# Performance work log

Hardware: AMD Instinct MI355X
Metric: run time of the kernel (lower is better)

Reference implementation:

```python
import jax, jax.numpy as jnp
import numpy as np

# hyperparams (match init_kwargs)
B, T, DV, DJ, L = 32, 256, 1024, 512, 20
K, S, LAYERS = 4, 2, 3
LAM = 4.0            # lambda_softmax used inside frame_by_word attention
MARGIN = 0.1         # opt.global_margin
EPS_BN = 1e-5
EPS_COS = 1e-8


def _bn(x):
    # training-mode BatchNorm1d(affine=False): per-channel stats over (batch, length)
    m = x.mean(axis=(0, 2), keepdims=True)
    v = ((x - m) ** 2).mean(axis=(0, 2), keepdims=True)
    return (x - m) / jnp.sqrt(v + EPS_BN)


def _conv1d(x, w, b, stride):
    # x: [N, Cin, L], w: [Cout, Cin, K], padding=0
    y = jax.lax.conv_general_dilated(x, w, (stride,), 'VALID',
                                     dimension_numbers=('NCH', 'OIH', 'NCH'))
    return y + b[None, :, None]


def setup_inputs() -> dict:
    key = jax.random.key(0)
    ks = jax.random.split(key, 10)
    inp = {
        'video': jax.random.normal(ks[0], (B, T, DV), jnp.float32),
        'words': jax.random.normal(ks[1], (B, L, DJ), jnp.float32),
        'w_masks': jnp.ones((B, L), jnp.float32),
        'conv0_w': jax.random.normal(ks[2], (DJ, DV, K), jnp.float32) * 0.02,
        'conv0_b': jnp.zeros((DJ,), jnp.float32),
        'conv1_w': jax.random.normal(ks[3], (DJ, DJ, K), jnp.float32) * 0.02,
        'conv1_b': jnp.zeros((DJ,), jnp.float32),
        'conv2_w': jax.random.normal(ks[4], (DJ, DJ, K), jnp.float32) * 0.02,
        'conv2_b': jnp.zeros((DJ,), jnp.float32),
        'conv1d_w': jax.random.normal(ks[5], (DJ, DJ, 1), jnp.float32) * 0.02,
        'conv1d_b': jnp.zeros((DJ,), jnp.float32),
    }
    return inp


def reference(video, words, w_masks, conv0_w, conv0_b, conv1_w, conv1_b,
              conv2_w, conv2_b, conv1d_w, conv1d_b):
    # --- conv/batchnorm feature extraction ---
    x = _bn(video.transpose(0, 2, 1))                     # [b, DV, T]
    feats = []
    for w_, b_ in ((conv0_w, conv0_b), (conv1_w, conv1_b), (conv2_w, conv2_b)):
        x = jax.nn.relu(_conv1d(x, w_, b_, S))
        feats.append(x)
    v = jnp.concatenate(feats, axis=-1)                   # [b, DJ, T']
    v = _conv1d(v, conv1d_w, conv1d_b, 1)
    v = _bn(v).transpose(0, 2, 1)                         # [b, T', DJ]
    w = _bn(words.transpose(0, 2, 1)).transpose(0, 2, 1)  # [b, L, DJ]

    # --- batched frame-by-word cross-attention over all (sentence i, video j) pairs ---
    att = jnp.einsum('jtd,ild->ijtl', v, w) * LAM         # [b_i, b_j, T', L]
    mask = (w_masks > 0.5)[:, None, None, :]
    att = jax.nn.softmax(jnp.where(mask, att, -1e9), axis=-1)
    v_s = jnp.einsum('ijtl,ild->ijtd', att, w)            # [b_i, b_j, T', DJ]

    # cosine similarity along feature dim
    num = jnp.einsum('jtd,ijtd->ijt', v, v_s)
    vn = jnp.maximum(jnp.linalg.norm(v, axis=-1), EPS_COS)[None]     # [1, b_j, T']
    vsn = jnp.maximum(jnp.linalg.norm(v_s, axis=-1), EPS_COS)        # [b_i, b_j, T']
    sim = num / (vn * vsn)                                # [b_i, b_j, T']

    b = sim.shape[0]
    idx = jnp.arange(b)
    positive_map = sim[idx, idx]                          # [b, T']
    scores = sim.max(axis=-1)                             # [b_i, b_j]

    # --- diag margin ranking loss ---
    dg = jnp.diagonal(scores)
    cost_s = jnp.clip(MARGIN + scores - dg[:, None], 0.0)
    cost_im = jnp.clip(MARGIN + scores - dg[None, :], 0.0)
    I = jnp.eye(b, dtype=bool)
    cost_s = jnp.where(I, 0.0, cost_s)
    cost_im = jnp.where(I, 0.0, cost_im)
    loss = cost_s.sum() / b + cost_im.sum() / b
    return loss, positive_map
```

## Files before the change

### kernel.cpp

```cpp
#include <hip/hip_runtime.h>
#include <math.h>

#define B_   32
#define T_   256
#define DV_  1024
#define DJ_  512
#define L_   20
#define T0_  127
#define T1_  62
#define T2_  30
#define TP_  219
#define LAM_ 4.0f
#define MARGIN_ 0.1f

typedef __attribute__((ext_vector_type(8))) short short8;
typedef __attribute__((ext_vector_type(4))) float f32x4;

static __device__ __forceinline__ unsigned short f2bf(float f) {
  union { float f; unsigned u; } v; v.f = f;
  unsigned r = v.u + 0x7fff + ((v.u >> 16) & 1);
  return (unsigned short)(r >> 16);
}

struct ushort4_t { unsigned short x, y, z, w; };

#define GLOAD_LDS16(gp, lp)                                                      \
  __builtin_amdgcn_global_load_lds(                                              \
      (const __attribute__((address_space(1))) void*)(gp),                       \
      (__attribute__((address_space(3))) void*)(lp), 16, 0, 0)

__global__ void reorder_all_k(const float* __restrict__ c0w, const float* __restrict__ c1w,
                              const float* __restrict__ c2w, const float* __restrict__ pww,
                              unsigned short* __restrict__ W0, unsigned short* __restrict__ W1,
                              unsigned short* __restrict__ W2, unsigned short* __restrict__ Wp) {
  int bid = blockIdx.x;
  if (bid < 2048) {
    int idx = bid * 256 + threadIdx.x;
    int co = idx >> 10, ci = idx & 1023;
    float4 w = *reinterpret_cast<const float4*>(c0w + (size_t)idx * 4);
    unsigned short* d = W0 + (size_t)co * 4096 + ci;
    d[0] = f2bf(w.x); d[1024] = f2bf(w.y); d[2048] = f2bf(w.z); d[3072] = f2bf(w.w);
  } else if (bid < 3072) {
    int idx = (bid - 2048) * 256 + threadIdx.x;
    int co = idx >> 9, ci = idx & 511;
    float4 w = *reinterpret_cast<const float4*>(c1w + (size_t)idx * 4);
    unsigned short* d = W1 + (size_t)co * 2048 + ci;
    d[0] = f2bf(w.x); d[512] = f2bf(w.y); d[1024] = f2bf(w.z); d[1536] = f2bf(w.w);
  } else if (bid < 4096) {
    int idx = (bid - 3072) * 256 + threadIdx.x;
    int co = idx >> 9, ci = idx & 511;
    float4 w = *reinterpret_cast<const float4*>(c2w + (size_t)idx * 4);
    unsigned short* d = W2 + (size_t)co * 2048 + ci;
    d[0] = f2bf(w.x); d[512] = f2bf(w.y); d[1024] = f2bf(w.z); d[1536] = f2bf(w.w);
  } else {
    int idx = (bid - 4096) * 256 + threadIdx.x;
    float4 v = *reinterpret_cast<const float4*>(pww + (size_t)idx * 4);
    ushort4_t h = { f2bf(v.x), f2bf(v.y), f2bf(v.z), f2bf(v.w) };
    reinterpret_cast<ushort4_t*>(Wp)[idx] = h;
  }
}

__global__ void stats1_k(const float* __restrict__ x, float* __restrict__ part,
                         int C, int rows, int rpg, int cpgShift) {
  int cpg  = 1 << cpgShift;
  int c4   = threadIdx.x & (cpg - 1);
  int rsub = threadIdx.x >> cpgShift;
  int nsub = 256 >> cpgShift;
  int r0 = blockIdx.x * rpg + rsub;
  int r1 = min(blockIdx.x * rpg + rpg, rows);
  float4 s = {0.f,0.f,0.f,0.f}, q = {0.f,0.f,0.f,0.f};
  for (int r = r0; r < r1; r += nsub) {
    float4 v = *reinterpret_cast<const float4*>(&x[(size_t)r * C + c4 * 4]);
    s.x += v.x; s.y += v.y; s.z += v.z; s.w += v.w;
    q.x += v.x*v.x; q.y += v.y*v.y; q.z += v.z*v.z; q.w += v.w*v.w;
  }
  float* ps = part + ((size_t)blockIdx.x * nsub + rsub) * 2 * C;
  reinterpret_cast<float4*>(ps)[c4] = s;
  reinterpret_cast<float4*>(ps + C)[c4] = q;
}

__global__ void stats2_k(const float* __restrict__ part, float* __restrict__ ms,
                         int C, int ng, float inv_n) {
  __shared__ float4 sS[8][33], sQ[8][33];
  int c4l = threadIdx.x & 31;
  int gs  = threadIdx.x >> 5;
  int c4  = blockIdx.x * 32 + c4l;
  float4 s = {0.f,0.f,0.f,0.f}, q = {0.f,0.f,0.f,0.f};
  for (int g = gs; g < ng; g += 8) {
    const float4* ps = reinterpret_cast<const float4*>(part + (size_t)g * 2 * C);
    float4 a = ps[c4];
    float4 b = ps[(C >> 2) + c4];
    s.x += a.x; s.y += a.y; s.z += a.z; s.w += a.w;
    q.x += b.x; q.y += b.y; q.z += b.z; q.w += b.w;
  }
  sS[gs][c4l] = s; sQ[gs][c4l] = q;
  __syncthreads();
  if (gs == 0) {
    float4 S = sS[0][c4l], Q = sQ[0][c4l];
#pragma unroll
    for (int k = 1; k < 8; ++k) {
      float4 a = sS[k][c4l], b = sQ[k][c4l];
      S.x += a.x; S.y += a.y; S.z += a.z; S.w += a.w;
      Q.x += b.x; Q.y += b.y; Q.z += b.z; Q.w += b.w;
    }
    int c = c4 * 4;
    float m0 = S.x * inv_n, m1 = S.y * inv_n, m2 = S.z * inv_n, m3 = S.w * inv_n;
    ms[c+0] = m0; ms[C+c+0] = rsqrtf(Q.x * inv_n - m0*m0 + 1e-5f);
    ms[c+1] = m1; ms[C+c+1] = rsqrtf(Q.y * inv_n - m1*m1 + 1e-5f);
    ms[c+2] = m2; ms[C+c+2] = rsqrtf(Q.z * inv_n - m2*m2 + 1e-5f);
    ms[c+3] = m3; ms[C+c+3] = rsqrtf(Q.w * inv_n - m3*m3 + 1e-5f);
  }
}

__global__ void vid_bn_cast_k(const float* __restrict__ video,
                              const float* __restrict__ ms,
                              unsigned short* __restrict__ vbf) {
  int i4 = blockIdx.x * 256 + threadIdx.x;
  float4 v = reinterpret_cast<const float4*>(video)[i4];
  int c = (i4 & 255) * 4;
  v.x = (v.x - ms[c+0]) * ms[1024+c+0];
  v.y = (v.y - ms[c+1]) * ms[1024+c+1];
  v.z = (v.z - ms[c+2]) * ms[1024+c+2];
  v.w = (v.w - ms[c+3]) * ms[1024+c+3];
  ushort4_t h = { f2bf(v.x), f2bf(v.y), f2bf(v.z), f2bf(v.w) };
  reinterpret_cast<ushort4_t*>(vbf)[i4] = h;
}

template<bool RELU, bool BIAS, bool OUT_BF16, bool PARTIAL>
__global__ __launch_bounds__(256) void mfma_gemm_k(
    const unsigned short* __restrict__ xin, const unsigned short* __restrict__ Wr,
    const float* __restrict__ bias, void* __restrict__ out,
    int b_stride, int row_off, int row_t_stride,
    int To, int M, int t_off_out, int ldout, int Ktot, int Kloc)
{
  __shared__ __align__(16) short As[2][64 * 32];
  __shared__ __align__(16) short Bs[2][64 * 32];

  const int tid  = threadIdx.x;
  const int lane = tid & 63;
  const int wv   = tid >> 6;
  const int wr   = wv >> 1;
  const int wc   = wv & 1;
  const int mbase = blockIdx.x * 64;
  const int nbase = blockIdx.y * 64;
  const int kstart = PARTIAL ? blockIdx.z * Kloc : 0;

  const int srow = tid >> 2;
  const int sb   = (((tid & 3) ^ ((srow ^ (srow >> 2)) & 3))) * 8;
  int ma = min(mbase + srow, M - 1);
  int b0 = ma / To, t0 = ma % To;
  const unsigned short* agp = xin + (size_t)b0 * b_stride + row_off
                              + (size_t)t0 * row_t_stride + sb + kstart;
  const unsigned short* bgp = Wr + (size_t)(nbase + srow) * Ktot + sb + kstart;

  f32x4 acc[2][2] = {};
  const int nsteps = Kloc >> 5;

#define STAGE(buf, k0)                                        \
  do {                                                        \
    GLOAD_LDS16(agp + (k0), &As[buf][wv * 512]);              \
    GLOAD_LDS16(bgp + (k0), &Bs[buf][wv * 512]);              \
  } while (0)

  STAGE(0, 0);
  __syncthreads();

  const int rsw   = (lane ^ (lane >> 2)) & 3;
  const int chunk = ((lane >> 4) ^ rsw) * 8;
  const int a_off = (wr * 32 + (lane & 15)) * 32 + chunk;
  const int b_off = (wc * 32 + (lane & 15)) * 32 + chunk;

  for (int s = 0; s < nsteps; ++s) {
    const int nb = s & 1;
    if (s + 1 < nsteps) STAGE(nb ^ 1, (s + 1) * 32);

    const short* Ab = &As[nb][a_off];
    const short* Bb = &Bs[nb][b_off];
    short8 af0 = *reinterpret_cast<const short8*>(Ab);
    short8 af1 = *reinterpret_cast<const short8*>(Ab + 512);
    short8 bf0 = *reinterpret_cast<const short8*>(Bb);
    short8 bf1 = *reinterpret_cast<const short8*>(Bb + 512);

    acc[0][0] = __builtin_amdgcn_mfma_f32_16x16x32_bf16(af0, bf0, acc[0][0], 0, 0, 0);
    acc[0][1] = __builtin_amdgcn_mfma_f32_16x16x32_bf16(af0, bf1, acc[0][1], 0, 0, 0);
    acc[1][0] = __builtin_amdgcn_mfma_f32_16x16x32_bf16(af1, bf0, acc[1][0], 0, 0, 0);
    acc[1][1] = __builtin_amdgcn_mfma_f32_16x16x32_bf16(af1, bf1, acc[1][1], 0, 0, 0);

    __syncthreads();
  }
#undef STAGE

  const int cl = lane & 15, rh = lane >> 4;
#pragma unroll
  for (int fm = 0; fm < 2; ++fm) {
#pragma unroll
    for (int fn = 0; fn < 2; ++fn) {
      int col = nbase + wc * 32 + fn * 16 + cl;
      float bv = BIAS ? bias[col] : 0.f;
      f32x4 v = acc[fm][fn];
#pragma unroll
      for (int r = 0; r < 4; ++r) {
        int m = mbase + wr * 32 + fm * 16 + rh * 4 + r;
        if (m < M) {
          if (PARTIAL) {
            float* pout = (float*)out + (size_t)blockIdx.z * ((size_t)M * ldout);
            pout[(size_t)m * ldout + col] = v[r];
          } else {
            int b = m / To, to = m % To;
            float x = v[r] + bv;
            if (RELU) x = fmaxf(x, 0.f);
            size_t oi = ((size_t)b * TP_ + t_off_out + to) * (size_t)ldout + col;
            if (OUT_BF16) ((unsigned short*)out)[oi] = f2bf(x);
            else          ((float*)out)[oi] = x;
          }
        }
      }
    }
  }
}

template<int S>
__global__ void reduce_conv_k(const float* __restrict__ part, const float* __restrict__ bias,
                              unsigned short* __restrict__ outb,
                              int M, int To, int t_off_out) {
  int idx = blockIdx.x * 256 + threadIdx.x;
  int m = idx >> 7, n4 = idx & 127;
  if (m >= M) return;
  size_t off = (size_t)m * 512 + n4 * 4;
  float4 a = *reinterpret_cast<const float4*>(part + off);
#pragma unroll
  for (int s = 1; s < S; ++s) {
    float4 b = *reinterpret_cast<const float4*>(part + (size_t)s * M * 512 + off);
    a.x += b.x; a.y += b.y; a.z += b.z; a.w += b.w;
  }
  float4 bv = *reinterpret_cast<const float4*>(bias + n4 * 4);
  a.x = fmaxf(a.x + bv.x, 0.f);
  a.y = fmaxf(a.y + bv.y, 0.f);
  a.z = fmaxf(a.z + bv.z, 0.f);
  a.w = fmaxf(a.w + bv.w, 0.f);
  int b_ = m / To, to = m % To;
  ushort4_t h = { f2bf(a.x), f2bf(a.y), f2bf(a.z), f2bf(a.w) };
  reinterpret_cast<ushort4_t*>(outb + ((size_t)b_ * TP_ + t_off_out + to) * 512)[n4] = h;
}

__global__ void v2_norm_vn_k(float* __restrict__ v2, const float* __restrict__ ms,
                             unsigned short* __restrict__ v2bf, float* __restrict__ vn) {
  int r = blockIdx.x, t = threadIdx.x;
  float* row = v2 + (size_t)r * DJ_;
  unsigned short* brow = v2bf + (size_t)r * DJ_;
  float ss = 0.f;
#pragma unroll
  for (int h = 0; h < 2; ++h) {
    int c4 = t + h * 64;
    float4 v = reinterpret_cast<float4*>(row)[c4];
    int c = c4 * 4;
    v.x = (v.x - ms[c+0]) * ms[DJ_+c+0];
    v.y = (v.y - ms[c+1]) * ms[DJ_+c+1];
    v.z = (v.z - ms[c+2]) * ms[DJ_+c+2];
    v.w = (v.w - ms[c+3]) * ms[DJ_+c+3];
    reinterpret_cast<float4*>(row)[c4] = v;
    ushort4_t h4 = { f2bf(v.x), f2bf(v.y), f2bf(v.z), f2bf(v.w) };
    reinterpret_cast<ushort4_t*>(brow)[c4] = h4;
    ss += v.x*v.x + v.y*v.y + v.z*v.z + v.w*v.w;
  }
#pragma unroll
  for (int o = 32; o; o >>= 1) ss += __shfl_down(ss, o, 64);
  if (t == 0) vn[r] = sqrtf(ss);
}

__global__ void wnorm_k(const float* __restrict__ words, const float* __restrict__ ms,
                        float* __restrict__ wbn, unsigned short* __restrict__ wbnb) {
  int idx = blockIdx.x * 256 + threadIdx.x;
  if (idx >= (B_ * L_ * DJ_) / 4) return;
  int c = (idx & 127) * 4;
  float4 v = reinterpret_cast<const float4*>(words)[idx];
  v.x = (v.x - ms[c+0]) * ms[DJ_+c+0];
  v.y = (v.y - ms[c+1]) * ms[DJ_+c+1];
  v.z = (v.z - ms[c+2]) * ms[DJ_+c+2];
  v.w = (v.w - ms[c+3]) * ms[DJ_+c+3];
  reinterpret_cast<float4*>(wbn)[idx] = v;
  ushort4_t h = { f2bf(v.x), f2bf(v.y), f2bf(v.z), f2bf(v.w) };
  reinterpret_cast<ushort4_t*>(wbnb)[idx] = h;
}

__global__ void gram_k(const float* __restrict__ wbn, float* __restrict__ G) {
  __shared__ float sw[L_ * 516];
  int i = blockIdx.x, tid = threadIdx.x;
  for (int idx = tid; idx < L_ * DJ_; idx += 256) {
    int l = idx >> 9, d = idx & 511;
    sw[l * 516 + d] = wbn[(size_t)i * L_ * DJ_ + idx];
  }
  __syncthreads();
  for (int p = tid; p < L_ * L_; p += 256) {
    int l = p / L_, l2 = p % L_;
    const float4* a = reinterpret_cast<const float4*>(&sw[l * 516]);
    const float4* b = reinterpret_cast<const float4*>(&sw[l2 * 516]);
    float acc = 0.f;
    for (int d4 = 0; d4 < 128; ++d4) {
      float4 av = a[d4], bv = b[d4];
      acc += av.x*bv.x + av.y*bv.y + av.z*bv.z + av.w*bv.w;
    }
    G[i * 400 + p] = acc;
  }
}

__global__ __launch_bounds__(256) void sim_k(
    const float* __restrict__ A, const float* __restrict__ G,
    const float* __restrict__ vn, const float* __restrict__ wmask,
    float* __restrict__ pos, float* __restrict__ scores) {
  int j = blockIdx.x, i = blockIdx.y;
  __shared__ float sG[400];
  __shared__ float sm[20];
  __shared__ float red[4];
  int tid = threadIdx.x;
  for (int p = tid; p < 400; p += 256) sG[p] = G[i * 400 + p];
  if (tid < 20) sm[tid] = wmask[i * 20 + tid];
  __syncthreads();

  float simv = -1e30f;
  if (tid < TP_) {
    const float* ar = A + ((size_t)j * TP_ + tid) * 640 + i * 20;
    float a[20], p[20];
    float mx = -1e30f;
#pragma unroll
    for (int l = 0; l < 20; ++l) {
      a[l] = ar[l];
      float lg = (sm[l] > 0.5f) ? LAM_ * a[l] : -1e9f;
      p[l] = lg;
      mx = fmaxf(mx, lg);
    }
    float Z = 0.f;
#pragma unroll
    for (int l = 0; l < 20; ++l) { p[l] = __expf(p[l] - mx); Z += p[l]; }
    float invZ = 1.f / Z, num = 0.f;
#pragma unroll
    for (int l = 0; l < 20; ++l) { p[l] *= invZ; num += p[l] * a[l]; }
    float q2 = 0.f;
#pragma unroll
    for (int l = 0; l < 20; ++l) {
      float gi = 0.f;
#pragma unroll
      for (int l2 = 0; l2 < 20; ++l2) gi += sG[l * 20 + l2] * p[l2];
      q2 += p[l] * gi;
    }
    float vnv = fmaxf(vn[(size_t)j * TP_ + tid], 1e-8f);
    float vsnv = fmaxf(sqrtf(q2), 1e-8f);
    simv = num / (vnv * vsnv);
    if (i == j) pos[i * TP_ + tid] = simv;
  }
  float mv = simv;
#pragma unroll
  for (int o = 32; o; o >>= 1) mv = fmaxf(mv, __shfl_down(mv, o, 64));
  if ((tid & 63) == 0) red[tid >> 6] = mv;
  __syncthreads();
  if (tid == 0)
    scores[i * 32 + j] = fmaxf(fmaxf(red[0], red[1]), fmaxf(red[2], red[3]));
}

__global__ void loss_k(const float* __restrict__ scores, float* __restrict__ out) {
  __shared__ float red[16];
  int tid = threadIdx.x;
  int i = tid >> 5, j = tid & 31;
  float s = scores[tid];
  float dgi = scores[i * 32 + i], dgj = scores[j * 32 + j];
  float c = 0.f;
  if (i != j)
    c = fmaxf(0.f, MARGIN_ + s - dgi) + fmaxf(0.f, MARGIN_ + s - dgj);
#pragma unroll
  for (int o = 32; o; o >>= 1) c += __shfl_down(c, o, 64);
  if ((tid & 63) == 0) red[tid >> 6] = c;
  __syncthreads();
  if (tid == 0) {
    float t = 0.f;
    for (int w = 0; w < 16; ++w) t += red[w];
    out[0] = t / 32.f;
  }
}

extern "C" void kernel_launch(void* const* d_in, const int* in_sizes, int n_in,
                              void* d_out, int out_size, void* d_ws, size_t ws_size,
                              hipStream_t stream) {
  const float* video = (const float*)d_in[0];
  const float* words = (const float*)d_in[1];
  const float* wmask = (const float*)d_in[2];
  const float* c0w = (const float*)d_in[3];
  const float* c0b = (const float*)d_in[4];
  const float* c1w = (const float*)d_in[5];
  const float* c1b = (const float*)d_in[6];
  const float* c2w = (const float*)d_in[7];
  const float* c2b = (const float*)d_in[8];
  const float* pww = (const float*)d_in[9];
  const float* pwb = (const float*)d_in[10];
  float* out = (float*)d_out;
  float* ws  = (float*)d_ws;

  float*          W0r    = ws;
  float*          W1r    = W0r + 1048576;
  float*          W2r    = W1r + 524288;
  float*          Wpw    = W2r + 524288;
  float*          AMvbf  = Wpw + 131072;
  float*          vcatb  = AMvbf + 4485120;
  float*          Pbuf   = vcatb + 1794048;
  float*          v2     = Pbuf;
  float*          v2bfp  = v2 + 3588096;
  float*          wbn    = v2bfp + 1794048;
  float*          wbnbp  = wbn + 327680;
  float*          G      = wbnbp + 163840;
  float*          vn     = G + 12800;
  float*          scores = vn + 7008;
  float*          vpart  = scores + 1024;
  float*          vms    = vpart + 1048576;
  float*          v2part = vms + 2048;
  float*          v2ms   = v2part + 897024;
  float*          wpart  = v2ms + 1024;
  float*          wms    = wpart + 81920;

  unsigned short* W0     = (unsigned short*)W0r;
  unsigned short* W1     = (unsigned short*)W1r;
  unsigned short* W2     = (unsigned short*)W2r;
  unsigned short* Wp     = (unsigned short*)Wpw;
  unsigned short* vbf    = (unsigned short*)AMvbf;
  float*          Amat   = AMvbf;
  unsigned short* vcb    = (unsigned short*)vcatb;
  unsigned short* v2bf   = (unsigned short*)v2bfp;
  unsigned short* wbnb   = (unsigned short*)wbnbp;

  reorder_all_k<<<4352, 256, 0, stream>>>(c0w, c1w, c2w, pww, W0, W1, W2, Wp);

  stats1_k<<<512, 256, 0, stream>>>(video, vpart, 1024, 8192, 16, 8);
  stats2_k<<<8, 256, 0, stream>>>(vpart, vms, 1024, 512, 1.f / 8192.f);
  vid_bn_cast_k<<<8192, 256, 0, stream>>>(video, vms, vbf);

  mfma_gemm_k<false, false, false, true><<<dim3(64, 8, 4), 256, 0, stream>>>(
      vbf, W0, nullptr, Pbuf, 262144, 0, 2048, T0_, 32 * T0_, 0, 512, 4096, 1024);
  reduce_conv_k<4><<<2032, 256, 0, stream>>>(Pbuf, c0b, vcb, 32 * T0_, T0_, 0);
  mfma_gemm_k<false, false, false, true><<<dim3(31, 8, 4), 256, 0, stream>>>(
      vcb, W1, nullptr, Pbuf, 112128, 0, 1024, T1_, 32 * T1_, 0, 512, 2048, 512);
  reduce_conv_k<4><<<992, 256, 0, stream>>>(Pbuf, c1b, vcb, 32 * T1_, T1_, T0_);
  mfma_gemm_k<false, false, false, true><<<dim3(15, 8, 8), 256, 0, stream>>>(
      vcb, W2, nullptr, Pbuf, 112128, 65024, 1024, T2_, 32 * T2_, 0, 512, 2048, 256);
  reduce_conv_k<8><<<480, 256, 0, stream>>>(Pbuf, c2b, vcb, 32 * T2_, T2_, T0_ + T1_);

  mfma_gemm_k<false, true, false, false><<<dim3(110, 8), 256, 0, stream>>>(
      vcb, Wp, pwb, v2, 112128, 0, 512, TP_, 32 * TP_, 0, 512, 512, 512);

  stats1_k<<<438, 256, 0, stream>>>(v2, v2part, 512, 7008, 16, 7);
  stats2_k<<<4, 256, 0, stream>>>(v2part, v2ms, 512, 876, 1.f / 7008.f);
  v2_norm_vn_k<<<7008, 64, 0, stream>>>(v2, v2ms, v2bf, vn);

  stats1_k<<<40, 256, 0, stream>>>(words, wpart, 512, 640, 16, 7);
  stats2_k<<<4, 256, 0, stream>>>(wpart, wms, 512, 80, 1.f / 640.f);
  wnorm_k<<<(81920 + 255) / 256, 256, 0, stream>>>(words, wms, wbn, wbnb);
  gram_k<<<32, 256, 0, stream>>>(wbn, G);

  mfma_gemm_k<false, false, false, false><<<dim3(110, 10), 256, 0, stream>>>(
      v2bf, wbnb, nullptr, Amat, 112128, 0, 512, TP_, 32 * TP_, 0, 640, 512, 512);

  sim_k<<<dim3(32, 32), 256, 0, stream>>>(Amat, G, vn, wmask, out + 1, scores);
  loss_k<<<1, 1024, 0, stream>>>(scores, out);
}
```

Before: 245.8 us.

## Enlarge MFMA GEMM tiles to 128x128 with 4x4 fragments per wave

```diff
diff --git a/kernel.cpp b/kernel.cpp
--- a/kernel.cpp
+++ b/kernel.cpp
@@ -133,42 +133,50 @@
     int b_stride, int row_off, int row_t_stride,
     int To, int M, int t_off_out, int ldout, int Ktot, int Kloc)
 {
-  __shared__ __align__(16) short As[2][64 * 32];
-  __shared__ __align__(16) short Bs[2][64 * 32];
+  __shared__ __align__(16) short As[2][128 * 32];
+  __shared__ __align__(16) short Bs[2][128 * 32];
 
   const int tid  = threadIdx.x;
   const int lane = tid & 63;
   const int wv   = tid >> 6;
   const int wr   = wv >> 1;
   const int wc   = wv & 1;
-  const int mbase = blockIdx.x * 64;
-  const int nbase = blockIdx.y * 64;
+  const int mbase = blockIdx.x * 128;
+  const int nbase = blockIdx.y * 128;
   const int kstart = PARTIAL ? blockIdx.z * Kloc : 0;
 
   const int srow = tid >> 2;
   const int sb   = (((tid & 3) ^ ((srow ^ (srow >> 2)) & 3))) * 8;
-  int ma = min(mbase + srow, M - 1);
-  int b0 = ma / To, t0 = ma % To;
-  const unsigned short* agp = xin + (size_t)b0 * b_stride + row_off
-                              + (size_t)t0 * row_t_stride + sb + kstart;
-  const unsigned short* bgp = Wr + (size_t)(nbase + srow) * Ktot + sb + kstart;
-
-  f32x4 acc[2][2] = {};
+  int ma0 = min(mbase + srow,      M - 1);
+  int ma1 = min(mbase + 64 + srow, M - 1);
+  int ba0 = ma0 / To, ta0 = ma0 % To;
+  int ba1 = ma1 / To, ta1 = ma1 % To;
+  const unsigned short* agp0 = xin + (size_t)ba0 * b_stride + row_off
+                               + (size_t)ta0 * row_t_stride + sb + kstart;
+  const unsigned short* agp1 = xin + (size_t)ba1 * b_stride + row_off
+                               + (size_t)ta1 * row_t_stride + sb + kstart;
+  const unsigned short* bgp0 = Wr + (size_t)(nbase + srow) * Ktot + sb + kstart;
+  const unsigned short* bgp1 = Wr + (size_t)(nbase + 64 + srow) * Ktot + sb + kstart;
+
+  f32x4 acc[4][4] = {};
   const int nsteps = Kloc >> 5;
 
 #define STAGE(buf, k0)                                        \
   do {                                                        \
-    GLOAD_LDS16(agp + (k0), &As[buf][wv * 512]);              \
-    GLOAD_LDS16(bgp + (k0), &Bs[buf][wv * 512]);              \
+    GLOAD_LDS16(agp0 + (k0), &As[buf][wv * 512]);             \
+    GLOAD_LDS16(agp1 + (k0), &As[buf][2048 + wv * 512]);      \
+    GLOAD_LDS16(bgp0 + (k0), &Bs[buf][wv * 512]);             \
+    GLOAD_LDS16(bgp1 + (k0), &Bs[buf][2048 + wv * 512]);      \
   } while (0)
 
   STAGE(0, 0);
   __syncthreads();
 
-  const int rsw   = (lane ^ (lane >> 2)) & 3;
+  const int l15   = lane & 15;
+  const int rsw   = (l15 ^ (l15 >> 2)) & 3;
   const int chunk = ((lane >> 4) ^ rsw) * 8;
-  const int a_off = (wr * 32 + (lane & 15)) * 32 + chunk;
-  const int b_off = (wc * 32 + (lane & 15)) * 32 + chunk;
+  const int a_off = (wr * 64 + l15) * 32 + chunk;
+  const int b_off = (wc * 64 + l15) * 32 + chunk;
 
   for (int s = 0; s < nsteps; ++s) {
     const int nb = s & 1;
@@ -176,15 +184,17 @@
 
     const short* Ab = &As[nb][a_off];
     const short* Bb = &Bs[nb][b_off];
-    short8 af0 = *reinterpret_cast<const short8*>(Ab);
-    short8 af1 = *reinterpret_cast<const short8*>(Ab + 512);
-    short8 bf0 = *reinterpret_cast<const short8*>(Bb);
-    short8 bf1 = *reinterpret_cast<const short8*>(Bb + 512);
-
-    acc[0][0] = __builtin_amdgcn_mfma_f32_16x16x32_bf16(af0, bf0, acc[0][0], 0, 0, 0);
-    acc[0][1] = __builtin_amdgcn_mfma_f32_16x16x32_bf16(af0, bf1, acc[0][1], 0, 0, 0);
-    acc[1][0] = __builtin_amdgcn_mfma_f32_16x16x32_bf16(af1, bf0, acc[1][0], 0, 0, 0);
-    acc[1][1] = __builtin_amdgcn_mfma_f32_16x16x32_bf16(af1, bf1, acc[1][1], 0, 0, 0);
+    short8 af[4], bf[4];
+#pragma unroll
+    for (int f = 0; f < 4; ++f) {
+      af[f] = *reinterpret_cast<const short8*>(Ab + f * 512);
+      bf[f] = *reinterpret_cast<const short8*>(Bb + f * 512);
+    }
+#pragma unroll
+    for (int fm = 0; fm < 4; ++fm)
+#pragma unroll
+      for (int fn = 0; fn < 4; ++fn)
+        acc[fm][fn] = __builtin_amdgcn_mfma_f32_16x16x32_bf16(af[fm], bf[fn], acc[fm][fn], 0, 0, 0);
 
     __syncthreads();
   }
@@ -192,15 +202,15 @@
 
   const int cl = lane & 15, rh = lane >> 4;
 #pragma unroll
-  for (int fm = 0; fm < 2; ++fm) {
-#pragma unroll
-    for (int fn = 0; fn < 2; ++fn) {
-      int col = nbase + wc * 32 + fn * 16 + cl;
+  for (int fm = 0; fm < 4; ++fm) {
+#pragma unroll
+    for (int fn = 0; fn < 4; ++fn) {
+      int col = nbase + wc * 64 + fn * 16 + cl;
       float bv = BIAS ? bias[col] : 0.f;
       f32x4 v = acc[fm][fn];
 #pragma unroll
       for (int r = 0; r < 4; ++r) {
-        int m = mbase + wr * 32 + fm * 16 + rh * 4 + r;
+        int m = mbase + wr * 64 + fm * 16 + rh * 4 + r;
         if (m < M) {
           if (PARTIAL) {
             float* pout = (float*)out + (size_t)blockIdx.z * ((size_t)M * ldout);
@@ -431,17 +441,17 @@
   stats2_k<<<8, 256, 0, stream>>>(vpart, vms, 1024, 512, 1.f / 8192.f);
   vid_bn_cast_k<<<8192, 256, 0, stream>>>(video, vms, vbf);
 
-  mfma_gemm_k<false, false, false, true><<<dim3(64, 8, 4), 256, 0, stream>>>(
+  mfma_gemm_k<false, false, false, true><<<dim3(32, 4, 4), 256, 0, stream>>>(
       vbf, W0, nullptr, Pbuf, 262144, 0, 2048, T0_, 32 * T0_, 0, 512, 4096, 1024);
   reduce_conv_k<4><<<2032, 256, 0, stream>>>(Pbuf, c0b, vcb, 32 * T0_, T0_, 0);
-  mfma_gemm_k<false, false, false, true><<<dim3(31, 8, 4), 256, 0, stream>>>(
-      vcb, W1, nullptr, Pbuf, 112128, 0, 1024, T1_, 32 * T1_, 0, 512, 2048, 512);
-  reduce_conv_k<4><<<992, 256, 0, stream>>>(Pbuf, c1b, vcb, 32 * T1_, T1_, T0_);
-  mfma_gemm_k<false, false, false, true><<<dim3(15, 8, 8), 256, 0, stream>>>(
+  mfma_gemm_k<false, false, false, true><<<dim3(16, 4, 8), 256, 0, stream>>>(
+      vcb, W1, nullptr, Pbuf, 112128, 0, 1024, T1_, 32 * T1_, 0, 512, 2048, 256);
+  reduce_conv_k<8><<<992, 256, 0, stream>>>(Pbuf, c1b, vcb, 32 * T1_, T1_, T0_);
+  mfma_gemm_k<false, false, false, true><<<dim3(8, 4, 8), 256, 0, stream>>>(
       vcb, W2, nullptr, Pbuf, 112128, 65024, 1024, T2_, 32 * T2_, 0, 512, 2048, 256);
   reduce_conv_k<8><<<480, 256, 0, stream>>>(Pbuf, c2b, vcb, 32 * T2_, T2_, T0_ + T1_);
 
-  mfma_gemm_k<false, true, false, false><<<dim3(110, 8), 256, 0, stream>>>(
+  mfma_gemm_k<false, true, false, false><<<dim3(55, 4), 256, 0, stream>>>(
       vcb, Wp, pwb, v2, 112128, 0, 512, TP_, 32 * TP_, 0, 512, 512, 512);
 
   stats1_k<<<438, 256, 0, stream>>>(v2, v2part, 512, 7008, 16, 7);
@@ -453,7 +463,7 @@
   wnorm_k<<<(81920 + 255) / 256, 256, 0, stream>>>(words, wms, wbn, wbnb);
   gram_k<<<32, 256, 0, stream>>>(wbn, G);
 
-  mfma_gemm_k<false, false, false, false><<<dim3(110, 10), 256, 0, stream>>>(
+  mfma_gemm_k<false, false, false, false><<<dim3(55, 5), 256, 0, stream>>>(
       v2bf, wbnb, nullptr, Amat, 112128, 0, 512, TP_, 32 * TP_, 0, 640, 512, 512);
 
   sim_k<<<dim3(32, 32), 256, 0, stream>>>(Amat, G, vn, wmask, out + 1, scores);
```

New measurement: 246.5 us. No clear change (+0.3%).
